# Kernel optimization log

Hardware: AMD Instinct MI355X
Metric: run time of the kernel (lower is better)

The kernel has to match this reference:

```python
import jax, jax.numpy as jnp
import numpy as np

ROPE_BASE = 10000.0

def _rope(x, positions):
    # x: [B, H, T, hs], rotate-half (GPT-NeoX style) rotary embedding
    hs = x.shape[-1]
    half = hs // 2
    inv_freq = 1.0 / (ROPE_BASE ** (jnp.arange(half, dtype=jnp.float32) / half))
    ang = positions.astype(jnp.float32)[:, None] * inv_freq[None, :]  # [T, half]
    cos, sin = jnp.cos(ang), jnp.sin(ang)
    x1, x2 = x[..., :half], x[..., half:]
    return jnp.concatenate([x1 * cos - x2 * sin, x1 * sin + x2 * cos], axis=-1)


def setup_inputs() -> dict:
    key = jax.random.key(0)
    ks = jax.random.split(key, 8)
    B, T, OFF, C, H = 1, 1024, 1024, 2048, 16
    hs = C // H
    return {
        "x": jax.random.normal(ks[0], (B, T, C), jnp.float32),
        "cached_k": jax.random.normal(ks[1], (B, H, OFF, hs), jnp.float32),
        "cached_v": jax.random.normal(ks[2], (B, H, OFF, hs), jnp.float32),
        "W_attn": jax.random.normal(ks[3], (C, 3 * C), jnp.float32) * 0.02,
        "b_attn": jnp.zeros((3 * C,), jnp.float32),
        "W_proj": jax.random.normal(ks[4], (C, C), jnp.float32) * 0.02,
        "b_proj": jnp.zeros((C,), jnp.float32),
        "decay_raw": jax.random.normal(ks[5], (16,), jnp.float32) * 0.5,
    }


def reference(x, cached_k, cached_v, W_attn, b_attn, W_proj, b_proj, decay_raw):
    B, T, C = x.shape
    H = decay_raw.shape[0]
    hs = C // H
    off = cached_k.shape[2]

    qkv = x @ W_attn + b_attn                       # [B, T, 3C]
    q, k, v = jnp.split(qkv, 3, axis=-1)
    to_heads = lambda t: t.reshape(B, T, H, hs).transpose(0, 2, 1, 3)  # [B,H,T,hs]
    q, k, v = to_heads(q), to_heads(k), to_heads(v)

    positions = jnp.arange(off, off + T)
    q = _rope(q, positions)
    k = _rope(k, positions)

    k = jnp.concatenate([cached_k, k], axis=2)      # [B, H, T_full, hs]
    v = jnp.concatenate([cached_v, v], axis=2)
    T_full = k.shape[2]

    # causal mask over full key length, offset for cache
    neg_inf = jnp.finfo(jnp.float32).min
    q_idx = positions                               # [T]
    k_idx = jnp.arange(T_full)                      # [T_full]
    causal = jnp.where(k_idx[None, :] > q_idx[:, None], neg_inf, 0.0)  # [T, T_full]

    # per-head distance-decay log-bias
    decay = jax.nn.softplus(decay_raw)              # [H]
    dist = jnp.maximum(q_idx[:, None] - k_idx[None, :], 0).astype(jnp.float32)
    logw = -jnp.log1p(decay[:, None, None] * jnp.log1p(dist))          # [H, T, T_full]
    bias = causal[None, :, :] + logw                # [H, T, T_full]

    scale = 1.0 / jnp.sqrt(jnp.float32(hs))
    scores = jnp.einsum('bhtd,bhsd->bhts', q, k) * scale + bias[None]
    attn = jax.nn.softmax(scores, axis=-1)
    y = jnp.einsum('bhts,bhsd->bhtd', attn, v)      # [B, H, T, hs]
    y = y.transpose(0, 2, 1, 3).reshape(B, T, C)
    y = y @ W_proj + b_proj
    return (y, k, v)
```

## Files before the change

kernel.cpp:

```cpp
#include <hip/hip_runtime.h>
#include <hip/hip_bf16.h>

typedef unsigned short u16;
typedef unsigned int u32;
typedef __attribute__((ext_vector_type(4))) float f32x4;
typedef __attribute__((ext_vector_type(8))) short bf16x8;

__device__ __forceinline__ u16 f2bf(float f) {
    union { float f; u32 u; } v; v.f = f;
    return (u16)((v.u + 0x7FFFu + ((v.u >> 16) & 1u)) >> 16);
}
__device__ __forceinline__ float bf2f(u16 b) {
    union { u32 u; float f; } v; v.u = ((u32)b) << 16;
    return v.f;
}
__device__ __forceinline__ void st_out(float* p, float v) { *p = v; }
__device__ __forceinline__ void st_out(u16* p, float v) { *p = f2bf(v); }

__device__ __forceinline__ f32x4 mfma16(bf16x8 a, bf16x8 b, f32x4 c) {
    return __builtin_amdgcn_mfma_f32_16x16x32_bf16(a, b, c, 0, 0, 0);
}

#define GLD_LDS16(g, l) __builtin_amdgcn_global_load_lds( \
    (const __attribute__((address_space(1))) void*)(g),   \
    (__attribute__((address_space(3))) void*)(l), 16, 0, 0)

__global__ __launch_bounds__(256) void k_prep(
    const float* __restrict__ W_attn, const float* __restrict__ W_proj,
    const float* __restrict__ x, const float* __restrict__ decay_raw,
    u16* __restrict__ WaT, u16* __restrict__ WpT, u16* __restrict__ Xb,
    float* __restrict__ bias_tab, float* __restrict__ cosT, float* __restrict__ sinT) {
    __shared__ float tile[64][65];
    const int b = blockIdx.x, tid = threadIdx.x;
    if (b < 4096) {
        const float* src; u16* dst; int R, Cc, bx, by;
        if (b < 3072) { src = W_attn; dst = WaT; R = 2048; Cc = 6144; bx = b % 96; by = b / 96; }
        else          { src = W_proj; dst = WpT; R = 2048; Cc = 2048; bx = (b - 3072) & 31; by = (b - 3072) >> 5; }
        int c0 = bx * 64, r0 = by * 64;
#pragma unroll
        for (int it = 0; it < 16; ++it) {
            int idx = it * 256 + tid;
            int r = idx >> 6, c = idx & 63;
            tile[r][c] = src[(size_t)(r0 + r) * Cc + c0 + c];
        }
        __syncthreads();
#pragma unroll
        for (int it = 0; it < 16; ++it) {
            int idx = it * 256 + tid;
            int cc = idx >> 6, rr = idx & 63;
            dst[(size_t)(c0 + cc) * R + r0 + rr] = f2bf(tile[rr][cc]);
        }
    } else if (b < 6144) {
        int i = (b - 4096) * 256 + tid;
        float4 v = ((const float4*)x)[i];
        u32 p0 = (u32)f2bf(v.x) | ((u32)f2bf(v.y) << 16);
        u32 p1 = (u32)f2bf(v.z) | ((u32)f2bf(v.w) << 16);
        uint2 p; p.x = p0; p.y = p1;
        *(uint2*)(Xb + (size_t)i * 4) = p;
    } else {
        int i = (b - 6144) * 256 + tid;
        if (i < 16 * 2048) {
            int h = i >> 11, dist = i & 2047;
            float dec = log1pf(expf(decay_raw[h]));
            bias_tab[i] = -log1pf(dec * log1pf((float)dist));
        }
        if (i < 1024 * 64) {
            int t = i >> 6, j = i & 63;
            float inv = expf(-logf(10000.0f) * (float)j / 64.0f);
            float ang = (float)(1024 + t) * inv;
            cosT[i] = cosf(ang);
            sinT[i] = sinf(ang);
        }
    }
}

template<int BM, int BN, int WRG, int WCG, typename OT>
__global__ __launch_bounds__(256) void k_gemm_bt(
    const u16* __restrict__ A, const u16* __restrict__ Bt,
    const float* __restrict__ bias, OT* __restrict__ C,
    int M, int N, int K) {
    constexpr int BK = 64;
    constexpr int WM = BM / WRG;
    constexpr int WN = BN / WCG;
    constexpr int MR = WM / 16;
    constexpr int NR = WN / 16;
    constexpr int LDSZ = (BM + BN) * BK * 2;
    __shared__ char lds[2][LDSZ];

    const int tid = threadIdx.x;
    const int lane = tid & 63, wid = tid >> 6;
    const int wr = wid / WCG, wc = wid % WCG;
    const int lhi = lane >> 4, llo = lane & 15;
    const int m0 = blockIdx.y * BM, n0 = blockIdx.x * BN;

    f32x4 acc[MR][NR];
#pragma unroll
    for (int m = 0; m < MR; ++m)
#pragma unroll
        for (int n = 0; n < NR; ++n)
            acc[m][n] = f32x4{0.f, 0.f, 0.f, 0.f};

    auto stage = [&](int buf, int k0) {
        char* ldsA = &lds[buf][0];
        char* ldsB = &lds[buf][0] + BM * BK * 2;
#pragma unroll
        for (int it = 0; it < (BM * 8) / 256; ++it) {
            int ci = it * 256 + wid * 64 + lane;
            int r = ci >> 3, c = ci & 7;
            int sc = c ^ (r & 7);
            GLD_LDS16(A + (size_t)(m0 + r) * K + k0 + sc * 8,
                      ldsA + (it * 256 + wid * 64) * 16);
        }
#pragma unroll
        for (int it = 0; it < (BN * 8) / 256; ++it) {
            int ci = it * 256 + wid * 64 + lane;
            int r = ci >> 3, c = ci & 7;
            int sc = c ^ (r & 7);
            GLD_LDS16(Bt + (size_t)(n0 + r) * K + k0 + sc * 8,
                      ldsB + (it * 256 + wid * 64) * 16);
        }
    };

    stage(0, 0);
    __syncthreads();
    int cur = 0;
    for (int k0 = 0; k0 < K; k0 += BK) {
        if (k0 + BK < K) stage(cur ^ 1, k0 + BK);
        const char* ldsA = &lds[cur][0];
        const char* ldsB = &lds[cur][0] + BM * BK * 2;
#pragma unroll
        for (int kk = 0; kk < BK; kk += 32) {
            bf16x8 af[MR], bfr[NR];
            const int clb = (kk >> 3) + lhi;
#pragma unroll
            for (int m = 0; m < MR; ++m) {
                int row = wr * WM + m * 16 + llo;
                af[m] = *(const bf16x8*)(ldsA + row * 128 + ((clb ^ (row & 7)) << 4));
            }
#pragma unroll
            for (int n = 0; n < NR; ++n) {
                int row = wc * WN + n * 16 + llo;
                bfr[n] = *(const bf16x8*)(ldsB + row * 128 + ((clb ^ (row & 7)) << 4));
            }
#pragma unroll
            for (int m = 0; m < MR; ++m)
#pragma unroll
                for (int n = 0; n < NR; ++n)
                    acc[m][n] = mfma16(af[m], bfr[n], acc[m][n]);
        }
        __syncthreads();
        cur ^= 1;
    }
#pragma unroll
    for (int m = 0; m < MR; ++m) {
        int row = m0 + wr * WM + m * 16 + lhi * 4;
#pragma unroll
        for (int n = 0; n < NR; ++n) {
            int col = n0 + wc * WN + n * 16 + llo;
            float bv = bias[col];
#pragma unroll
            for (int j = 0; j < 4; ++j)
                st_out(&C[(size_t)(row + j) * N + col], acc[m][n][j] + bv);
        }
    }
}

__global__ void k_fuse2(const u16* __restrict__ qkv,
                        const float* __restrict__ cosT, const float* __restrict__ sinT,
                        const float* __restrict__ cached_k,
                        u16* __restrict__ qb, u16* __restrict__ kb,
                        float* __restrict__ out_k) {
    const int b = blockIdx.x;
    if (b < 4096) {
        int i = b * 256 + threadIdx.x;
        int j = i & 63;
        int t = (i >> 6) & 1023;
        int h = i >> 16;
        const u16* row = qkv + (size_t)t * 6144;
        float q1 = bf2f(row[h * 128 + j]),        q2 = bf2f(row[h * 128 + j + 64]);
        float k1 = bf2f(row[2048 + h * 128 + j]), k2 = bf2f(row[2048 + h * 128 + j + 64]);
        float cv = cosT[t * 64 + j], sv = sinT[t * 64 + j];
        float qo1 = q1 * cv - q2 * sv, qo2 = q1 * sv + q2 * cv;
        float ko1 = k1 * cv - k2 * sv, ko2 = k1 * sv + k2 * cv;
        size_t qoff = ((size_t)h * 1024 + t) * 128 + j;
        qb[qoff] = f2bf(qo1); qb[qoff + 64] = f2bf(qo2);
        size_t koff = ((size_t)h * 2048 + 1024 + t) * 128 + j;
        kb[koff] = f2bf(ko1); kb[koff + 64] = f2bf(ko2);
        out_k[koff] = ko1; out_k[koff + 64] = ko2;
    } else {
        int i = (b - 4096) * 256 + threadIdx.x;
        int d = i & 127, s = (i >> 7) & 1023, h = i >> 17;
        float v = cached_k[i];
        size_t off = ((size_t)h * 2048 + s) * 128 + d;
        out_k[off] = v;
        kb[off] = f2bf(v);
    }
}

__global__ __launch_bounds__(256) void k_v_assemble(
    const float* __restrict__ cached_v, const u16* __restrict__ qkv,
    float* __restrict__ out_v, u16* __restrict__ vt) {
    __shared__ u16 tile[64][65];
    int s0 = blockIdx.x * 64, d0 = blockIdx.y * 64, h = blockIdx.z;
    int tid = threadIdx.x;
#pragma unroll
    for (int it = 0; it < 16; ++it) {
        int idx = it * 256 + tid;
        int r = idx >> 6, c = idx & 63;
        int s = s0 + r, d = d0 + c;
        u16 v = (s < 1024)
            ? f2bf(cached_v[((size_t)h * 1024 + s) * 128 + d])
            : qkv[(size_t)(s - 1024) * 6144 + 4096 + h * 128 + d];
        tile[r][c] = v;
        out_v[((size_t)h * 2048 + s) * 128 + d] = bf2f(v);
    }
    __syncthreads();
#pragma unroll
    for (int it = 0; it < 16; ++it) {
        int idx = it * 256 + tid;
        int dd = idx >> 6, ss = idx & 63;
        vt[((size_t)h * 128 + d0 + dd) * 2048 + s0 + ss] = tile[ss][dd];
    }
}

__global__ __launch_bounds__(256, 4) void k_attn(
    const u16* __restrict__ qb,
    const u16* __restrict__ kb,
    const u16* __restrict__ vt,
    const float* __restrict__ bias_tab,
    u16* __restrict__ Pacc,
    float* __restrict__ Pm,
    float* __restrict__ Pl) {
    __shared__ char ldsK[2][32 * 256];
    __shared__ char ldsV[2][128 * 64];
    __shared__ u16 ldsP[4][16 * 36];

    const int bid = blockIdx.x;
    const int xcd = bid & 7, idx = bid >> 3;
    const int work = xcd * 128 + idx;
    const int h = work >> 6, rem = work & 63;
    const int qt = rem >> 2, chunk = rem & 3;
    const int qbase = qt * 64;
    const int tid = threadIdx.x, lane = tid & 63, wid = tid >> 6;
    const int lhi = lane >> 4, llo = lane & 15;
    const int slot = (h * 16 + qt) * 4 + chunk;

    const u16* kg = kb + (size_t)h * 2048 * 128;
    const u16* vg = vt + (size_t)h * 128 * 2048;
    const float* bt = bias_tab + h * 2048;

    bf16x8 qf[4];
    {
        const u16* qrow = qb + ((size_t)h * 1024 + qbase + wid * 16 + llo) * 128;
#pragma unroll
        for (int c = 0; c < 4; ++c)
            qf[c] = *(const bf16x8*)(qrow + c * 32 + lhi * 8);
    }

    f32x4 acc[8];
#pragma unroll
    for (int d = 0; d < 8; ++d) acc[d] = f32x4{0.f, 0.f, 0.f, 0.f};
    float mrow[4] = {-3e38f, -3e38f, -3e38f, -3e38f};
    float lrow[4] = {0.f, 0.f, 0.f, 0.f};

    const int ntiles = 34 + 2 * qt;
    const float scale = 0.08838834764831845f;
    const int qpos = 1024 + qbase + wid * 16 + lhi * 4;

    auto stage = [&](int b, int st) {
        int sbase = st * 32;
#pragma unroll
        for (int it = 0; it < 2; ++it) {
            int ci = it * 256 + tid;
            int r = ci >> 4, c = ci & 15;
            int sc = c ^ (r & 7);
            GLD_LDS16(kg + (size_t)(sbase + r) * 128 + sc * 8,
                      &ldsK[b][0] + (it * 256 + wid * 64) * 16);
        }
#pragma unroll
        for (int it = 0; it < 2; ++it) {
            int ci = it * 256 + tid;
            int r = ci >> 2, c = ci & 3;
            int sc = c ^ ((r >> 1) & 3);
            GLD_LDS16(vg + (size_t)r * 2048 + sbase + sc * 8,
                      &ldsV[b][0] + (it * 256 + wid * 64) * 16);
        }
    };

    const int st0 = chunk + 4 * ((ntiles - 1 - chunk) >> 2);
    stage(0, st0);
    __syncthreads();
    int cur = 0;
    for (int st = st0; st >= chunk; st -= 4) {
        if (st >= chunk + 4) stage(cur ^ 1, st - 4);
        const int sbase = st * 32;
        const char* lK = &ldsK[cur][0];
        const char* lV = &ldsV[cur][0];

        f32x4 sc4[2];
        __builtin_amdgcn_s_setprio(1);
#pragma unroll
        for (int sub = 0; sub < 2; ++sub) {
            f32x4 s4 = f32x4{0.f, 0.f, 0.f, 0.f};
            int key = sub * 16 + llo;
#pragma unroll
            for (int c2 = 0; c2 < 4; ++c2) {
                int cl = c2 * 4 + lhi;
                bf16x8 kf = *(const bf16x8*)(lK + key * 256 + ((cl ^ (key & 7)) << 4));
                s4 = mfma16(qf[c2], kf, s4);
            }
            sc4[sub] = s4;
        }
        __builtin_amdgcn_s_setprio(0);

#pragma unroll
        for (int sub = 0; sub < 2; ++sub) {
            int key = sbase + sub * 16 + llo;
#pragma unroll
            for (int j = 0; j < 4; ++j) {
                int dist = qpos + j - key;
                float bv = bt[dist < 0 ? 0 : dist];
                sc4[sub][j] = (dist < 0) ? -3e38f : sc4[sub][j] * scale + bv;
            }
        }
        float tmax[4];
        int ok = 1;
#pragma unroll
        for (int j = 0; j < 4; ++j) {
            tmax[j] = fmaxf(sc4[0][j], sc4[1][j]);
            ok &= (tmax[j] <= mrow[j] + 8.0f) ? 1 : 0;
        }
        if (!__all(ok)) {
#pragma unroll
            for (int j = 0; j < 4; ++j) {
                float t = tmax[j];
                t = fmaxf(t, __shfl_xor(t, 1));
                t = fmaxf(t, __shfl_xor(t, 2));
                t = fmaxf(t, __shfl_xor(t, 4));
                t = fmaxf(t, __shfl_xor(t, 8));
                float mnew = fmaxf(mrow[j], t);
                float fs = __expf(mrow[j] - mnew);
                mrow[j] = mnew;
                lrow[j] *= fs;
#pragma unroll
                for (int d = 0; d < 8; ++d) acc[d][j] *= fs;
            }
        }
#pragma unroll
        for (int sub = 0; sub < 2; ++sub)
#pragma unroll
            for (int j = 0; j < 4; ++j) {
                float p = __expf(sc4[sub][j] - mrow[j]);
                sc4[sub][j] = p;
                lrow[j] += p;
            }

        u16* P = &ldsP[wid][0];
#pragma unroll
        for (int sub = 0; sub < 2; ++sub)
#pragma unroll
            for (int j = 0; j < 4; ++j)
                P[(lhi * 4 + j) * 36 + sub * 16 + llo] = f2bf(sc4[sub][j]);

        bf16x8 pf = *(const bf16x8*)((const char*)P + llo * 72 + lhi * 16);
        __builtin_amdgcn_s_setprio(1);
#pragma unroll
        for (int db = 0; db < 8; ++db) {
            int dr = db * 16 + llo;
            int cl = lhi ^ ((dr >> 1) & 3);
            bf16x8 vf = *(const bf16x8*)(lV + dr * 64 + cl * 16);
            acc[db] = mfma16(pf, vf, acc[db]);
        }
        __builtin_amdgcn_s_setprio(0);
        __syncthreads();
        cur ^= 1;
    }

#pragma unroll
    for (int j = 0; j < 4; ++j) {
        float t = lrow[j];
        t += __shfl_xor(t, 1);
        t += __shfl_xor(t, 2);
        t += __shfl_xor(t, 4);
        t += __shfl_xor(t, 8);
        lrow[j] = t;
    }

    if (llo == 0) {
#pragma unroll
        for (int j = 0; j < 4; ++j) {
            int r = wid * 16 + lhi * 4 + j;
            Pm[(size_t)slot * 64 + r] = mrow[j];
            Pl[(size_t)slot * 64 + r] = lrow[j];
        }
    }
#pragma unroll
    for (int db = 0; db < 8; ++db)
#pragma unroll
        for (int j = 0; j < 4; ++j) {
            int r = wid * 16 + lhi * 4 + j;
            Pacc[(size_t)slot * 8192 + r * 128 + db * 16 + llo] = f2bf(acc[db][j]);
        }
}

__global__ __launch_bounds__(256) void k_merge(
    const u16* __restrict__ Pacc, const float* __restrict__ Pm,
    const float* __restrict__ Pl, u16* __restrict__ yb) {
    const int b = blockIdx.x;
    const int h = b >> 6, qt = (b >> 2) & 15, quarter = b & 3;
    const int slot0 = (h * 16 + qt) * 4;
    const int tid = threadIdx.x;
    const int r = tid >> 2, dd = (tid & 3) * 8 + quarter * 32;

    float m[4], l[4];
#pragma unroll
    for (int c = 0; c < 4; ++c) {
        m[c] = Pm[(size_t)(slot0 + c) * 64 + r];
        l[c] = Pl[(size_t)(slot0 + c) * 64 + r];
    }
    float M = fmaxf(fmaxf(m[0], m[1]), fmaxf(m[2], m[3]));
    float w[4], L = 0.f;
#pragma unroll
    for (int c = 0; c < 4; ++c) {
        w[c] = __expf(m[c] - M);
        L += w[c] * l[c];
    }
    float inv = 1.0f / L;

    float y[8];
#pragma unroll
    for (int i = 0; i < 8; ++i) y[i] = 0.f;
#pragma unroll
    for (int c = 0; c < 4; ++c) {
        const uint4* pa = (const uint4*)(Pacc + (size_t)(slot0 + c) * 8192 + r * 128 + dd);
        float wc = w[c];
        uint4 v = *pa;
        u32 a[4] = {v.x, v.y, v.z, v.w};
#pragma unroll
        for (int p = 0; p < 4; ++p) {
            y[p * 2]     += wc * bf2f((u16)(a[p] & 0xFFFF));
            y[p * 2 + 1] += wc * bf2f((u16)(a[p] >> 16));
        }
    }
    int trow = qt * 64 + r;
    uint4 outv;
    u32* ow = (u32*)&outv;
#pragma unroll
    for (int k = 0; k < 4; ++k)
        ow[k] = (u32)f2bf(y[2 * k] * inv) | ((u32)f2bf(y[2 * k + 1] * inv) << 16);
    *(uint4*)(yb + (size_t)trow * 2048 + h * 128 + dd) = outv;
}

extern "C" void kernel_launch(void* const* d_in, const int* in_sizes, int n_in,
                              void* d_out, int out_size, void* d_ws, size_t ws_size,
                              hipStream_t stream) {
    (void)in_sizes; (void)n_in; (void)out_size;
    const float* x         = (const float*)d_in[0];
    const float* cached_k  = (const float*)d_in[1];
    const float* cached_v  = (const float*)d_in[2];
    const float* W_attn    = (const float*)d_in[3];
    const float* b_attn    = (const float*)d_in[4];
    const float* W_proj    = (const float*)d_in[5];
    const float* b_proj    = (const float*)d_in[6];
    const float* decay_raw = (const float*)d_in[7];

    float* out_y = (float*)d_out;
    float* out_k = out_y + 2097152;
    float* out_v = out_y + 6291456;

    char* ws = (char*)d_ws;
    if (ws_size < 63569920) return;
    u16*   WaT  = (u16*)(ws);
    u16*   WpT  = (u16*)(ws + 25165824);
    u16*   Xb   = (u16*)(ws + 33554432);
    u16*   QKVb = (u16*)(ws + 37748736);
    float* BT   = (float*)(ws + 62914560);
    float* CT   = (float*)(ws + 63045632);
    float* ST   = (float*)(ws + 63307776);
    u16*   Qb   = (u16*)(ws);
    u16*   Kb   = (u16*)(ws + 4194304);
    u16*   Vt   = (u16*)(ws + 12582912);
    u16*   Yb   = (u16*)(ws + 20971520);
    float* Pm   = (float*)(ws + 33554432);
    float* Pl   = (float*)(ws + 33816576);
    u16*   Pacc = (u16*)(ws + 37748736);

    k_prep<<<6400, 256, 0, stream>>>(W_attn, W_proj, x, decay_raw, WaT, WpT, Xb, BT, CT, ST);
    k_gemm_bt<128, 64, 2, 2, u16><<<dim3(96, 8), 256, 0, stream>>>(Xb, WaT, b_attn, QKVb, 1024, 6144, 2048);
    k_fuse2<<<12288, 256, 0, stream>>>(QKVb, CT, ST, cached_k, Qb, Kb, out_k);
    k_v_assemble<<<dim3(32, 2, 16), 256, 0, stream>>>(cached_v, QKVb, out_v, Vt);
    k_attn<<<1024, 256, 0, stream>>>(Qb, Kb, Vt, BT, Pacc, Pm, Pl);
    k_merge<<<1024, 256, 0, stream>>>(Pacc, Pm, Pl, Yb);
    k_gemm_bt<64, 64, 2, 2, float><<<dim3(32, 16), 256, 0, stream>>>(Yb, WpT, b_proj, out_y, 1024, 2048, 2048);
}
```

Baseline: 139.4 us.

## Split attention into six key chunks, fold scale into Q, prefetch bias, use exp2

The attention kernel now splits each query tile's key range into six interleaved chunks instead of four, launching 1536 blocks for more parallelism, and the merge kernel combines six partials. The softmax scale and log2(e) are folded into Q in the rope kernel and into the bias table, so the inner loop uses exp2f and skips a multiply. Bias values for fully unmasked tiles are prefetched one iteration ahead as vector loads instead of being gathered per element, and the rescale threshold is adjusted for the base-2 domain. The extra chunks add more partial-result traffic and merge work, and the Pl workspace offset moves to fit the larger Pm.

```diff
diff --git a/kernel.cpp b/kernel.cpp
--- a/kernel.cpp
+++ b/kernel.cpp
@@ -4,6 +4,7 @@
 typedef unsigned short u16;
 typedef unsigned int u32;
 typedef __attribute__((ext_vector_type(4))) float f32x4;
+typedef float f32x4u __attribute__((ext_vector_type(4), aligned(4)));
 typedef __attribute__((ext_vector_type(8))) short bf16x8;
 
 __device__ __forceinline__ u16 f2bf(float f) {
@@ -24,6 +25,9 @@
 #define GLD_LDS16(g, l) __builtin_amdgcn_global_load_lds( \
     (const __attribute__((address_space(1))) void*)(g),   \
     (__attribute__((address_space(3))) void*)(l), 16, 0, 0)
+
+#define LOG2E 1.4426950408889634f
+#define QSCALE 0.12751743f
 
 __global__ __launch_bounds__(256) void k_prep(
     const float* __restrict__ W_attn, const float* __restrict__ W_proj,
@@ -62,7 +66,7 @@
         if (i < 16 * 2048) {
             int h = i >> 11, dist = i & 2047;
             float dec = log1pf(expf(decay_raw[h]));
-            bias_tab[i] = -log1pf(dec * log1pf((float)dist));
+            bias_tab[i] = -log1pf(dec * log1pf((float)dist)) * LOG2E;
         }
         if (i < 1024 * 64) {
             int t = i >> 6, j = i & 63;
@@ -183,7 +187,7 @@
         float qo1 = q1 * cv - q2 * sv, qo2 = q1 * sv + q2 * cv;
         float ko1 = k1 * cv - k2 * sv, ko2 = k1 * sv + k2 * cv;
         size_t qoff = ((size_t)h * 1024 + t) * 128 + j;
-        qb[qoff] = f2bf(qo1); qb[qoff + 64] = f2bf(qo2);
+        qb[qoff] = f2bf(qo1 * QSCALE); qb[qoff + 64] = f2bf(qo2 * QSCALE);
         size_t koff = ((size_t)h * 2048 + 1024 + t) * 128 + j;
         kb[koff] = f2bf(ko1); kb[koff + 64] = f2bf(ko2);
         out_k[koff] = ko1; out_k[koff + 64] = ko2;
@@ -237,13 +241,13 @@
 
     const int bid = blockIdx.x;
     const int xcd = bid & 7, idx = bid >> 3;
-    const int work = xcd * 128 + idx;
-    const int h = work >> 6, rem = work & 63;
-    const int qt = rem >> 2, chunk = rem & 3;
+    const int work = xcd * 192 + idx;
+    const int h = work / 96, rem = work % 96;
+    const int qt = rem / 6, chunk = rem % 6;
     const int qbase = qt * 64;
     const int tid = threadIdx.x, lane = tid & 63, wid = tid >> 6;
     const int lhi = lane >> 4, llo = lane & 15;
-    const int slot = (h * 16 + qt) * 4 + chunk;
+    const int slot = (h * 16 + qt) * 6 + chunk;
 
     const u16* kg = kb + (size_t)h * 2048 * 128;
     const u16* vg = vt + (size_t)h * 128 * 2048;
@@ -264,7 +268,6 @@
     float lrow[4] = {0.f, 0.f, 0.f, 0.f};
 
     const int ntiles = 34 + 2 * qt;
-    const float scale = 0.08838834764831845f;
     const int qpos = 1024 + qbase + wid * 16 + lhi * 4;
 
     auto stage = [&](int b, int st) {
@@ -287,15 +290,26 @@
         }
     };
 
-    const int st0 = chunk + 4 * ((ntiles - 1 - chunk) >> 2);
+    f32x4u bpre0, bpre1;
+    auto pf_bias = [&](int st) {
+        int d0 = qpos - (st * 32 + llo);
+        int d1 = d0 - 16;
+        bpre0 = *(const f32x4u*)(bt + (d0 < 0 ? 0 : d0));
+        bpre1 = *(const f32x4u*)(bt + (d1 < 0 ? 0 : d1));
+    };
+
+    const int st0 = chunk + 6 * ((ntiles - 1 - chunk) / 6);
     stage(0, st0);
+    pf_bias(st0);
     __syncthreads();
     int cur = 0;
-    for (int st = st0; st >= chunk; st -= 4) {
-        if (st >= chunk + 4) stage(cur ^ 1, st - 4);
+    for (int st = st0; st >= chunk; st -= 6) {
+        if (st >= chunk + 6) stage(cur ^ 1, st - 6);
         const int sbase = st * 32;
         const char* lK = &ldsK[cur][0];
         const char* lV = &ldsV[cur][0];
+        f32x4u bc0 = bpre0, bc1 = bpre1;
+        if (st >= chunk + 6) pf_bias(st - 6);
 
         f32x4 sc4[2];
         __builtin_amdgcn_s_setprio(1);
@@ -313,14 +327,22 @@
         }
         __builtin_amdgcn_s_setprio(0);
 
-#pragma unroll
-        for (int sub = 0; sub < 2; ++sub) {
-            int key = sbase + sub * 16 + llo;
+        if (sbase + 31 <= 1024 + qbase + wid * 16) {
 #pragma unroll
             for (int j = 0; j < 4; ++j) {
-                int dist = qpos + j - key;
-                float bv = bt[dist < 0 ? 0 : dist];
-                sc4[sub][j] = (dist < 0) ? -3e38f : sc4[sub][j] * scale + bv;
+                sc4[0][j] += bc0[j];
+                sc4[1][j] += bc1[j];
+            }
+        } else {
+#pragma unroll
+            for (int sub = 0; sub < 2; ++sub) {
+                int key = sbase + sub * 16 + llo;
+#pragma unroll
+                for (int j = 0; j < 4; ++j) {
+                    int dist = qpos + j - key;
+                    float bv = bt[dist < 0 ? 0 : dist];
+                    sc4[sub][j] = (dist < 0) ? -3e38f : sc4[sub][j] + bv;
+                }
             }
         }
         float tmax[4];
@@ -328,7 +350,7 @@
 #pragma unroll
         for (int j = 0; j < 4; ++j) {
             tmax[j] = fmaxf(sc4[0][j], sc4[1][j]);
-            ok &= (tmax[j] <= mrow[j] + 8.0f) ? 1 : 0;
+            ok &= (tmax[j] <= mrow[j] + 11.5416f) ? 1 : 0;
         }
         if (!__all(ok)) {
 #pragma unroll
@@ -339,7 +361,7 @@
                 t = fmaxf(t, __shfl_xor(t, 4));
                 t = fmaxf(t, __shfl_xor(t, 8));
                 float mnew = fmaxf(mrow[j], t);
-                float fs = __expf(mrow[j] - mnew);
+                float fs = exp2f(mrow[j] - mnew);
                 mrow[j] = mnew;
                 lrow[j] *= fs;
 #pragma unroll
@@ -350,7 +372,7 @@
         for (int sub = 0; sub < 2; ++sub)
 #pragma unroll
             for (int j = 0; j < 4; ++j) {
-                float p = __expf(sc4[sub][j] - mrow[j]);
+                float p = exp2f(sc4[sub][j] - mrow[j]);
                 sc4[sub][j] = p;
                 lrow[j] += p;
             }
@@ -408,21 +430,23 @@
     const float* __restrict__ Pl, u16* __restrict__ yb) {
     const int b = blockIdx.x;
     const int h = b >> 6, qt = (b >> 2) & 15, quarter = b & 3;
-    const int slot0 = (h * 16 + qt) * 4;
+    const int slot0 = (h * 16 + qt) * 6;
     const int tid = threadIdx.x;
     const int r = tid >> 2, dd = (tid & 3) * 8 + quarter * 32;
 
-    float m[4], l[4];
-#pragma unroll
-    for (int c = 0; c < 4; ++c) {
+    float m[6], l[6];
+#pragma unroll
+    for (int c = 0; c < 6; ++c) {
         m[c] = Pm[(size_t)(slot0 + c) * 64 + r];
         l[c] = Pl[(size_t)(slot0 + c) * 64 + r];
     }
-    float M = fmaxf(fmaxf(m[0], m[1]), fmaxf(m[2], m[3]));
-    float w[4], L = 0.f;
-#pragma unroll
-    for (int c = 0; c < 4; ++c) {
-        w[c] = __expf(m[c] - M);
+    float M = m[0];
+#pragma unroll
+    for (int c = 1; c < 6; ++c) M = fmaxf(M, m[c]);
+    float w[6], L = 0.f;
+#pragma unroll
+    for (int c = 0; c < 6; ++c) {
+        w[c] = exp2f(m[c] - M);
         L += w[c] * l[c];
     }
     float inv = 1.0f / L;
@@ -431,7 +455,7 @@
 #pragma unroll
     for (int i = 0; i < 8; ++i) y[i] = 0.f;
 #pragma unroll
-    for (int c = 0; c < 4; ++c) {
+    for (int c = 0; c < 6; ++c) {
         const uint4* pa = (const uint4*)(Pacc + (size_t)(slot0 + c) * 8192 + r * 128 + dd);
         float wc = w[c];
         uint4 v = *pa;
@@ -482,14 +506,14 @@
     u16*   Vt   = (u16*)(ws + 12582912);
     u16*   Yb   = (u16*)(ws + 20971520);
     float* Pm   = (float*)(ws + 33554432);
-    float* Pl   = (float*)(ws + 33816576);
+    float* Pl   = (float*)(ws + 33947648);
     u16*   Pacc = (u16*)(ws + 37748736);
 
     k_prep<<<6400, 256, 0, stream>>>(W_attn, W_proj, x, decay_raw, WaT, WpT, Xb, BT, CT, ST);
     k_gemm_bt<128, 64, 2, 2, u16><<<dim3(96, 8), 256, 0, stream>>>(Xb, WaT, b_attn, QKVb, 1024, 6144, 2048);
     k_fuse2<<<12288, 256, 0, stream>>>(QKVb, CT, ST, cached_k, Qb, Kb, out_k);
     k_v_assemble<<<dim3(32, 2, 16), 256, 0, stream>>>(cached_v, QKVb, out_v, Vt);
-    k_attn<<<1024, 256, 0, stream>>>(Qb, Kb, Vt, BT, Pacc, Pm, Pl);
+    k_attn<<<1536, 256, 0, stream>>>(Qb, Kb, Vt, BT, Pacc, Pm, Pl);
     k_merge<<<1024, 256, 0, stream>>>(Pacc, Pm, Pl, Yb);
     k_gemm_bt<64, 64, 2, 2, float><<<dim3(32, 16), 256, 0, stream>>>(Yb, WpT, b_proj, out_y, 1024, 2048, 2048);
 }
```

Result: no change. 142.2 us (+2.0%).

## Restructure attention kernel to two-wave blocks with transposed QK and register P

Applied to the files above, without the earlier changes.

The attention kernel now runs 128-thread blocks where each wave handles 32 query rows (two 16-row MFMA tiles). This reuses each K/V fragment loaded from LDS across two MFMAs. QK^T is computed transposed so each lane owns a query row, and P is packed to bf16 in registers and permuted with cross-lane shuffles instead of going through LDS. The softmax scale and log2e are folded into Q and the bias table so exp2 can be used, and fully unmasked tiles load the distance bias as vectors. The cost is higher register pressure and fewer waves per block, which could reduce occupancy.

```diff
diff --git a/kernel.cpp b/kernel.cpp
--- a/kernel.cpp
+++ b/kernel.cpp
@@ -4,6 +4,7 @@
 typedef unsigned short u16;
 typedef unsigned int u32;
 typedef __attribute__((ext_vector_type(4))) float f32x4;
+typedef float f32x4u __attribute__((ext_vector_type(4), aligned(4)));
 typedef __attribute__((ext_vector_type(8))) short bf16x8;
 
 __device__ __forceinline__ u16 f2bf(float f) {
@@ -20,10 +21,18 @@
 __device__ __forceinline__ f32x4 mfma16(bf16x8 a, bf16x8 b, f32x4 c) {
     return __builtin_amdgcn_mfma_f32_16x16x32_bf16(a, b, c, 0, 0, 0);
 }
+__device__ __forceinline__ u32 cvt_pk_bf16(float lo, float hi) {
+    u32 r;
+    asm("v_cvt_pk_bf16_f32 %0, %1, %2" : "=v"(r) : "v"(lo), "v"(hi));
+    return r;
+}
 
 #define GLD_LDS16(g, l) __builtin_amdgcn_global_load_lds( \
     (const __attribute__((address_space(1))) void*)(g),   \
     (__attribute__((address_space(3))) void*)(l), 16, 0, 0)
+
+#define LOG2E 1.4426950408889634f
+#define QSCALE 0.12751743f
 
 __global__ __launch_bounds__(256) void k_prep(
     const float* __restrict__ W_attn, const float* __restrict__ W_proj,
@@ -62,7 +71,7 @@
         if (i < 16 * 2048) {
             int h = i >> 11, dist = i & 2047;
             float dec = log1pf(expf(decay_raw[h]));
-            bias_tab[i] = -log1pf(dec * log1pf((float)dist));
+            bias_tab[i] = -log1pf(dec * log1pf((float)dist)) * LOG2E;
         }
         if (i < 1024 * 64) {
             int t = i >> 6, j = i & 63;
@@ -183,7 +192,7 @@
         float qo1 = q1 * cv - q2 * sv, qo2 = q1 * sv + q2 * cv;
         float ko1 = k1 * cv - k2 * sv, ko2 = k1 * sv + k2 * cv;
         size_t qoff = ((size_t)h * 1024 + t) * 128 + j;
-        qb[qoff] = f2bf(qo1); qb[qoff + 64] = f2bf(qo2);
+        qb[qoff] = f2bf(qo1 * QSCALE); qb[qoff + 64] = f2bf(qo2 * QSCALE);
         size_t koff = ((size_t)h * 2048 + 1024 + t) * 128 + j;
         kb[koff] = f2bf(ko1); kb[koff + 64] = f2bf(ko2);
         out_k[koff] = ko1; out_k[koff + 64] = ko2;
@@ -223,7 +232,7 @@
     }
 }
 
-__global__ __launch_bounds__(256, 4) void k_attn(
+__global__ __launch_bounds__(128, 2) void k_attn(
     const u16* __restrict__ qb,
     const u16* __restrict__ kb,
     const u16* __restrict__ vt,
@@ -233,7 +242,6 @@
     float* __restrict__ Pl) {
     __shared__ char ldsK[2][32 * 256];
     __shared__ char ldsV[2][128 * 64];
-    __shared__ u16 ldsP[4][16 * 36];
 
     const int bid = blockIdx.x;
     const int xcd = bid & 7, idx = bid >> 3;
@@ -249,42 +257,59 @@
     const u16* vg = vt + (size_t)h * 128 * 2048;
     const float* bt = bias_tab + h * 2048;
 
-    bf16x8 qf[4];
-    {
-        const u16* qrow = qb + ((size_t)h * 1024 + qbase + wid * 16 + llo) * 128;
+    bf16x8 qf[2][4];
+#pragma unroll
+    for (int m = 0; m < 2; ++m) {
+        const u16* qrow = qb + ((size_t)h * 1024 + qbase + wid * 32 + m * 16 + llo) * 128;
 #pragma unroll
         for (int c = 0; c < 4; ++c)
-            qf[c] = *(const bf16x8*)(qrow + c * 32 + lhi * 8);
-    }
-
-    f32x4 acc[8];
-#pragma unroll
-    for (int d = 0; d < 8; ++d) acc[d] = f32x4{0.f, 0.f, 0.f, 0.f};
-    float mrow[4] = {-3e38f, -3e38f, -3e38f, -3e38f};
-    float lrow[4] = {0.f, 0.f, 0.f, 0.f};
+            qf[m][c] = *(const bf16x8*)(qrow + c * 32 + lhi * 8);
+    }
+
+    f32x4 acc[2][8];
+#pragma unroll
+    for (int m = 0; m < 2; ++m)
+#pragma unroll
+        for (int d = 0; d < 8; ++d) acc[m][d] = f32x4{0.f, 0.f, 0.f, 0.f};
+    float mrow[2] = {-3e38f, -3e38f};
+    float lrow[2] = {0.f, 0.f};
 
     const int ntiles = 34 + 2 * qt;
-    const float scale = 0.08838834764831845f;
-    const int qpos = 1024 + qbase + wid * 16 + lhi * 4;
+    const int qpos0 = 1024 + qbase + wid * 32 + llo;
 
     auto stage = [&](int b, int st) {
         int sbase = st * 32;
 #pragma unroll
-        for (int it = 0; it < 2; ++it) {
-            int ci = it * 256 + tid;
+        for (int it = 0; it < 4; ++it) {
+            int ci = it * 128 + tid;
             int r = ci >> 4, c = ci & 15;
             int sc = c ^ (r & 7);
             GLD_LDS16(kg + (size_t)(sbase + r) * 128 + sc * 8,
-                      &ldsK[b][0] + (it * 256 + wid * 64) * 16);
-        }
-#pragma unroll
-        for (int it = 0; it < 2; ++it) {
-            int ci = it * 256 + tid;
+                      &ldsK[b][0] + (it * 128 + wid * 64) * 16);
+        }
+#pragma unroll
+        for (int it = 0; it < 4; ++it) {
+            int ci = it * 128 + tid;
             int r = ci >> 2, c = ci & 3;
             int sc = c ^ ((r >> 1) & 3);
             GLD_LDS16(vg + (size_t)r * 2048 + sbase + sc * 8,
-                      &ldsV[b][0] + (it * 256 + wid * 64) * 16);
-        }
+                      &ldsV[b][0] + (it * 128 + wid * 64) * 16);
+        }
+    };
+
+    auto permP = [&](u32 p0, u32 p1, u32 p2, u32 p3) -> bf16x8 {
+        u32 r16a = (u32)__shfl_xor((int)(lhi == 1 ? p0 : p2), 16);
+        u32 r16b = (u32)__shfl_xor((int)(lhi == 1 ? p1 : p3), 16);
+        u32 r32a = (u32)__shfl_xor((int)(lhi == 3 ? p0 : p2), 32);
+        u32 r32b = (u32)__shfl_xor((int)(lhi == 3 ? p1 : p3), 32);
+        u32 r48a = (u32)__shfl_xor((int)(lhi == 2 ? p0 : p2), 48);
+        u32 r48b = (u32)__shfl_xor((int)(lhi == 2 ? p1 : p3), 48);
+        union { u32 w[4]; bf16x8 v; } u;
+        u.w[0] = lhi == 0 ? p0 : lhi == 1 ? r48a : lhi == 2 ? r32a : r16a;
+        u.w[1] = lhi == 0 ? p1 : lhi == 1 ? r48b : lhi == 2 ? r32b : r16b;
+        u.w[2] = lhi == 0 ? r16a : lhi == 1 ? r32a : lhi == 2 ? r48a : p2;
+        u.w[3] = lhi == 0 ? r16b : lhi == 1 ? r32b : lhi == 2 ? r48b : p3;
+        return u.v;
     };
 
     const int st0 = chunk + 4 * ((ntiles - 1 - chunk) >> 2);
@@ -297,79 +322,111 @@
         const char* lK = &ldsK[cur][0];
         const char* lV = &ldsV[cur][0];
 
-        f32x4 sc4[2];
+        const int D0 = qpos0 - sbase - lhi * 4;
+        f32x4u wB = *(const f32x4u*)(bt + (D0 - 3 < 0 ? 0 : D0 - 3));
+        f32x4u wA = *(const f32x4u*)(bt + (D0 + 13 < 0 ? 0 : D0 + 13));
+        f32x4u wC = *(const f32x4u*)(bt + (D0 - 19 < 0 ? 0 : D0 - 19));
+
+        f32x4 sc4[2][2];
         __builtin_amdgcn_s_setprio(1);
 #pragma unroll
         for (int sub = 0; sub < 2; ++sub) {
-            f32x4 s4 = f32x4{0.f, 0.f, 0.f, 0.f};
+            f32x4 a0 = f32x4{0.f, 0.f, 0.f, 0.f};
+            f32x4 a1 = f32x4{0.f, 0.f, 0.f, 0.f};
             int key = sub * 16 + llo;
 #pragma unroll
             for (int c2 = 0; c2 < 4; ++c2) {
                 int cl = c2 * 4 + lhi;
                 bf16x8 kf = *(const bf16x8*)(lK + key * 256 + ((cl ^ (key & 7)) << 4));
-                s4 = mfma16(qf[c2], kf, s4);
+                a0 = mfma16(kf, qf[0][c2], a0);
+                a1 = mfma16(kf, qf[1][c2], a1);
             }
-            sc4[sub] = s4;
+            sc4[0][sub] = a0;
+            sc4[1][sub] = a1;
         }
         __builtin_amdgcn_s_setprio(0);
 
-#pragma unroll
-        for (int sub = 0; sub < 2; ++sub) {
-            int key = sbase + sub * 16 + llo;
+        if (sbase + 31 <= 1024 + qbase + wid * 32) {
 #pragma unroll
             for (int j = 0; j < 4; ++j) {
-                int dist = qpos + j - key;
-                float bv = bt[dist < 0 ? 0 : dist];
-                sc4[sub][j] = (dist < 0) ? -3e38f : sc4[sub][j] * scale + bv;
+                sc4[0][0][j] += wB[3 - j];
+                sc4[0][1][j] += wC[3 - j];
+                sc4[1][0][j] += wA[3 - j];
+                sc4[1][1][j] += wB[3 - j];
             }
-        }
-        float tmax[4];
+        } else {
+#pragma unroll
+            for (int m = 0; m < 2; ++m)
+#pragma unroll
+                for (int sub = 0; sub < 2; ++sub)
+#pragma unroll
+                    for (int j = 0; j < 4; ++j) {
+                        int key = sbase + sub * 16 + lhi * 4 + j;
+                        int dist = qpos0 + m * 16 - key;
+                        float bv = bt[dist < 0 ? 0 : dist];
+                        sc4[m][sub][j] = (dist < 0) ? -3e38f : sc4[m][sub][j] + bv;
+                    }
+        }
+
+        float tmax[2];
         int ok = 1;
 #pragma unroll
-        for (int j = 0; j < 4; ++j) {
-            tmax[j] = fmaxf(sc4[0][j], sc4[1][j]);
-            ok &= (tmax[j] <= mrow[j] + 8.0f) ? 1 : 0;
+        for (int m = 0; m < 2; ++m) {
+            float t = fmaxf(fmaxf(fmaxf(sc4[m][0][0], sc4[m][0][1]),
+                                  fmaxf(sc4[m][0][2], sc4[m][0][3])),
+                            fmaxf(fmaxf(sc4[m][1][0], sc4[m][1][1]),
+                                  fmaxf(sc4[m][1][2], sc4[m][1][3])));
+            tmax[m] = t;
+            ok &= (t <= mrow[m] + 11.5416f) ? 1 : 0;
         }
         if (!__all(ok)) {
 #pragma unroll
-            for (int j = 0; j < 4; ++j) {
-                float t = tmax[j];
-                t = fmaxf(t, __shfl_xor(t, 1));
-                t = fmaxf(t, __shfl_xor(t, 2));
-                t = fmaxf(t, __shfl_xor(t, 4));
-                t = fmaxf(t, __shfl_xor(t, 8));
-                float mnew = fmaxf(mrow[j], t);
-                float fs = __expf(mrow[j] - mnew);
-                mrow[j] = mnew;
-                lrow[j] *= fs;
-#pragma unroll
-                for (int d = 0; d < 8; ++d) acc[d][j] *= fs;
+            for (int m = 0; m < 2; ++m) {
+                float t = tmax[m];
+                t = fmaxf(t, __shfl_xor(t, 16));
+                t = fmaxf(t, __shfl_xor(t, 32));
+                float mnew = fmaxf(mrow[m], t);
+                float fs = exp2f(mrow[m] - mnew);
+                mrow[m] = mnew;
+                lrow[m] *= fs;
+                float fsj[4];
+#pragma unroll
+                for (int j = 0; j < 4; ++j)
+                    fsj[j] = __shfl(fs, ((lane >> 4) << 2) + j);
+#pragma unroll
+                for (int d = 0; d < 8; ++d)
+#pragma unroll
+                    for (int j = 0; j < 4; ++j) acc[m][d][j] *= fsj[j];
             }
         }
-#pragma unroll
-        for (int sub = 0; sub < 2; ++sub)
-#pragma unroll
-            for (int j = 0; j < 4; ++j) {
-                float p = __expf(sc4[sub][j] - mrow[j]);
-                sc4[sub][j] = p;
-                lrow[j] += p;
-            }
-
-        u16* P = &ldsP[wid][0];
-#pragma unroll
-        for (int sub = 0; sub < 2; ++sub)
-#pragma unroll
-            for (int j = 0; j < 4; ++j)
-                P[(lhi * 4 + j) * 36 + sub * 16 + llo] = f2bf(sc4[sub][j]);
-
-        bf16x8 pf = *(const bf16x8*)((const char*)P + llo * 72 + lhi * 16);
+
+        bf16x8 pa[2];
+#pragma unroll
+        for (int m = 0; m < 2; ++m) {
+            float p[8];
+#pragma unroll
+            for (int sub = 0; sub < 2; ++sub)
+#pragma unroll
+                for (int j = 0; j < 4; ++j) {
+                    float e = exp2f(sc4[m][sub][j] - mrow[m]);
+                    lrow[m] += e;
+                    p[sub * 4 + j] = e;
+                }
+            u32 pk0 = cvt_pk_bf16(p[0], p[1]);
+            u32 pk1 = cvt_pk_bf16(p[2], p[3]);
+            u32 pk2 = cvt_pk_bf16(p[4], p[5]);
+            u32 pk3 = cvt_pk_bf16(p[6], p[7]);
+            pa[m] = permP(pk0, pk1, pk2, pk3);
+        }
+
         __builtin_amdgcn_s_setprio(1);
 #pragma unroll
         for (int db = 0; db < 8; ++db) {
             int dr = db * 16 + llo;
             int cl = lhi ^ ((dr >> 1) & 3);
             bf16x8 vf = *(const bf16x8*)(lV + dr * 64 + cl * 16);
-            acc[db] = mfma16(pf, vf, acc[db]);
+            acc[0][db] = mfma16(pa[0], vf, acc[0][db]);
+            acc[1][db] = mfma16(pa[1], vf, acc[1][db]);
         }
         __builtin_amdgcn_s_setprio(0);
         __syncthreads();
@@ -377,30 +434,30 @@
     }
 
 #pragma unroll
-    for (int j = 0; j < 4; ++j) {
-        float t = lrow[j];
-        t += __shfl_xor(t, 1);
-        t += __shfl_xor(t, 2);
-        t += __shfl_xor(t, 4);
-        t += __shfl_xor(t, 8);
-        lrow[j] = t;
-    }
-
-    if (llo == 0) {
-#pragma unroll
-        for (int j = 0; j < 4; ++j) {
-            int r = wid * 16 + lhi * 4 + j;
-            Pm[(size_t)slot * 64 + r] = mrow[j];
-            Pl[(size_t)slot * 64 + r] = lrow[j];
-        }
-    }
-#pragma unroll
-    for (int db = 0; db < 8; ++db)
-#pragma unroll
-        for (int j = 0; j < 4; ++j) {
-            int r = wid * 16 + lhi * 4 + j;
-            Pacc[(size_t)slot * 8192 + r * 128 + db * 16 + llo] = f2bf(acc[db][j]);
-        }
+    for (int m = 0; m < 2; ++m) {
+        float t = lrow[m];
+        t += __shfl_xor(t, 16);
+        t += __shfl_xor(t, 32);
+        lrow[m] = t;
+    }
+
+    if (lhi == 0) {
+#pragma unroll
+        for (int m = 0; m < 2; ++m) {
+            int r = wid * 32 + m * 16 + llo;
+            Pm[(size_t)slot * 64 + r] = mrow[m];
+            Pl[(size_t)slot * 64 + r] = lrow[m];
+        }
+    }
+#pragma unroll
+    for (int m = 0; m < 2; ++m)
+#pragma unroll
+        for (int db = 0; db < 8; ++db)
+#pragma unroll
+            for (int j = 0; j < 4; ++j) {
+                int r = wid * 32 + m * 16 + lhi * 4 + j;
+                Pacc[(size_t)slot * 8192 + r * 128 + db * 16 + llo] = f2bf(acc[m][db][j]);
+            }
 }
 
 __global__ __launch_bounds__(256) void k_merge(
@@ -422,7 +479,7 @@
     float w[4], L = 0.f;
 #pragma unroll
     for (int c = 0; c < 4; ++c) {
-        w[c] = __expf(m[c] - M);
+        w[c] = exp2f(m[c] - M);
         L += w[c] * l[c];
     }
     float inv = 1.0f / L;
@@ -489,7 +546,7 @@
     k_gemm_bt<128, 64, 2, 2, u16><<<dim3(96, 8), 256, 0, stream>>>(Xb, WaT, b_attn, QKVb, 1024, 6144, 2048);
     k_fuse2<<<12288, 256, 0, stream>>>(QKVb, CT, ST, cached_k, Qb, Kb, out_k);
     k_v_assemble<<<dim3(32, 2, 16), 256, 0, stream>>>(cached_v, QKVb, out_v, Vt);
-    k_attn<<<1024, 256, 0, stream>>>(Qb, Kb, Vt, BT, Pacc, Pm, Pl);
+    k_attn<<<1024, 128, 0, stream>>>(Qb, Kb, Vt, BT, Pacc, Pm, Pl);
     k_merge<<<1024, 256, 0, stream>>>(Pacc, Pm, Pl, Yb);
     k_gemm_bt<64, 64, 2, 2, float><<<dim3(32, 16), 256, 0, stream>>>(Yb, WpT, b_proj, out_y, 1024, 2048, 2048);
 }
```

New measurement: 140.7 us. No clear change (+0.9%).

## Transpose QK MFMA to keep P in registers and use exp2 softmax

Applied to the files above, without the earlier changes.

Swaps the operands of the QK^T MFMA so each lane holds one query row. Row max and sum then need only cross-group shuffles, and the P matrix is rebuilt for the PV MFMA with lane shuffles and packed bf16 converts instead of an LDS round trip. The softmax scale and log2e are folded into Q and the bias table so exp2 can be used. Unmasked tiles load the bias as contiguous vector reads instead of per-element gathers. The shuffle-based permutation adds VALU and cross-lane work, and prescaling Q before bf16 rounding slightly changes numerics.

```diff
diff --git a/kernel.cpp b/kernel.cpp
--- a/kernel.cpp
+++ b/kernel.cpp
@@ -4,6 +4,7 @@
 typedef unsigned short u16;
 typedef unsigned int u32;
 typedef __attribute__((ext_vector_type(4))) float f32x4;
+typedef float f32x4u __attribute__((ext_vector_type(4), aligned(4)));
 typedef __attribute__((ext_vector_type(8))) short bf16x8;
 
 __device__ __forceinline__ u16 f2bf(float f) {
@@ -20,10 +21,18 @@
 __device__ __forceinline__ f32x4 mfma16(bf16x8 a, bf16x8 b, f32x4 c) {
     return __builtin_amdgcn_mfma_f32_16x16x32_bf16(a, b, c, 0, 0, 0);
 }
+__device__ __forceinline__ u32 cvt_pk_bf16(float lo, float hi) {
+    u32 r;
+    asm("v_cvt_pk_bf16_f32 %0, %1, %2" : "=v"(r) : "v"(lo), "v"(hi));
+    return r;
+}
 
 #define GLD_LDS16(g, l) __builtin_amdgcn_global_load_lds( \
     (const __attribute__((address_space(1))) void*)(g),   \
     (__attribute__((address_space(3))) void*)(l), 16, 0, 0)
+
+#define LOG2E 1.4426950408889634f
+#define QSCALE 0.12751743f
 
 __global__ __launch_bounds__(256) void k_prep(
     const float* __restrict__ W_attn, const float* __restrict__ W_proj,
@@ -62,7 +71,7 @@
         if (i < 16 * 2048) {
             int h = i >> 11, dist = i & 2047;
             float dec = log1pf(expf(decay_raw[h]));
-            bias_tab[i] = -log1pf(dec * log1pf((float)dist));
+            bias_tab[i] = -log1pf(dec * log1pf((float)dist)) * LOG2E;
         }
         if (i < 1024 * 64) {
             int t = i >> 6, j = i & 63;
@@ -183,7 +192,7 @@
         float qo1 = q1 * cv - q2 * sv, qo2 = q1 * sv + q2 * cv;
         float ko1 = k1 * cv - k2 * sv, ko2 = k1 * sv + k2 * cv;
         size_t qoff = ((size_t)h * 1024 + t) * 128 + j;
-        qb[qoff] = f2bf(qo1); qb[qoff + 64] = f2bf(qo2);
+        qb[qoff] = f2bf(qo1 * QSCALE); qb[qoff + 64] = f2bf(qo2 * QSCALE);
         size_t koff = ((size_t)h * 2048 + 1024 + t) * 128 + j;
         kb[koff] = f2bf(ko1); kb[koff + 64] = f2bf(ko2);
         out_k[koff] = ko1; out_k[koff + 64] = ko2;
@@ -233,7 +242,6 @@
     float* __restrict__ Pl) {
     __shared__ char ldsK[2][32 * 256];
     __shared__ char ldsV[2][128 * 64];
-    __shared__ u16 ldsP[4][16 * 36];
 
     const int bid = blockIdx.x;
     const int xcd = bid & 7, idx = bid >> 3;
@@ -260,12 +268,11 @@
     f32x4 acc[8];
 #pragma unroll
     for (int d = 0; d < 8; ++d) acc[d] = f32x4{0.f, 0.f, 0.f, 0.f};
-    float mrow[4] = {-3e38f, -3e38f, -3e38f, -3e38f};
-    float lrow[4] = {0.f, 0.f, 0.f, 0.f};
+    float mrow = -3e38f;
+    float lrow = 0.f;
 
     const int ntiles = 34 + 2 * qt;
-    const float scale = 0.08838834764831845f;
-    const int qpos = 1024 + qbase + wid * 16 + lhi * 4;
+    const int qpos = 1024 + qbase + wid * 16 + llo;
 
     auto stage = [&](int b, int st) {
         int sbase = st * 32;
@@ -285,6 +292,21 @@
             GLD_LDS16(vg + (size_t)r * 2048 + sbase + sc * 8,
                       &ldsV[b][0] + (it * 256 + wid * 64) * 16);
         }
+    };
+
+    auto permP = [&](u32 p0, u32 p1, u32 p2, u32 p3) -> bf16x8 {
+        u32 r16a = (u32)__shfl_xor((int)(lhi == 1 ? p0 : p2), 16);
+        u32 r16b = (u32)__shfl_xor((int)(lhi == 1 ? p1 : p3), 16);
+        u32 r32a = (u32)__shfl_xor((int)(lhi == 3 ? p0 : p2), 32);
+        u32 r32b = (u32)__shfl_xor((int)(lhi == 3 ? p1 : p3), 32);
+        u32 r48a = (u32)__shfl_xor((int)(lhi == 2 ? p0 : p2), 48);
+        u32 r48b = (u32)__shfl_xor((int)(lhi == 2 ? p1 : p3), 48);
+        union { u32 w[4]; bf16x8 v; } u;
+        u.w[0] = lhi == 0 ? p0 : lhi == 1 ? r48a : lhi == 2 ? r32a : r16a;
+        u.w[1] = lhi == 0 ? p1 : lhi == 1 ? r48b : lhi == 2 ? r32b : r16b;
+        u.w[2] = lhi == 0 ? r16a : lhi == 1 ? r32a : lhi == 2 ? r48a : p2;
+        u.w[3] = lhi == 0 ? r16b : lhi == 1 ? r32b : lhi == 2 ? r48b : p3;
+        return u.v;
     };
 
     const int st0 = chunk + 4 * ((ntiles - 1 - chunk) >> 2);
@@ -297,6 +319,10 @@
         const char* lK = &ldsK[cur][0];
         const char* lV = &ldsV[cur][0];
 
+        const int D0 = qpos - sbase - lhi * 4;
+        f32x4u wB = *(const f32x4u*)(bt + (D0 - 3 < 0 ? 0 : D0 - 3));
+        f32x4u wC = *(const f32x4u*)(bt + (D0 - 19 < 0 ? 0 : D0 - 19));
+
         f32x4 sc4[2];
         __builtin_amdgcn_s_setprio(1);
 #pragma unroll
@@ -307,92 +333,87 @@
             for (int c2 = 0; c2 < 4; ++c2) {
                 int cl = c2 * 4 + lhi;
                 bf16x8 kf = *(const bf16x8*)(lK + key * 256 + ((cl ^ (key & 7)) << 4));
-                s4 = mfma16(qf[c2], kf, s4);
+                s4 = mfma16(kf, qf[c2], s4);
             }
             sc4[sub] = s4;
         }
         __builtin_amdgcn_s_setprio(0);
 
-#pragma unroll
-        for (int sub = 0; sub < 2; ++sub) {
-            int key = sbase + sub * 16 + llo;
+        if (sbase + 31 <= 1024 + qbase + wid * 16) {
 #pragma unroll
             for (int j = 0; j < 4; ++j) {
-                int dist = qpos + j - key;
-                float bv = bt[dist < 0 ? 0 : dist];
-                sc4[sub][j] = (dist < 0) ? -3e38f : sc4[sub][j] * scale + bv;
+                sc4[0][j] += wB[3 - j];
+                sc4[1][j] += wC[3 - j];
             }
-        }
-        float tmax[4];
-        int ok = 1;
-#pragma unroll
-        for (int j = 0; j < 4; ++j) {
-            tmax[j] = fmaxf(sc4[0][j], sc4[1][j]);
-            ok &= (tmax[j] <= mrow[j] + 8.0f) ? 1 : 0;
-        }
+        } else {
+#pragma unroll
+            for (int sub = 0; sub < 2; ++sub)
+#pragma unroll
+                for (int j = 0; j < 4; ++j) {
+                    int key = sbase + sub * 16 + lhi * 4 + j;
+                    int dist = qpos - key;
+                    float bv = bt[dist < 0 ? 0 : dist];
+                    sc4[sub][j] = (dist < 0) ? -3e38f : sc4[sub][j] + bv;
+                }
+        }
+
+        float tmax = fmaxf(fmaxf(fmaxf(sc4[0][0], sc4[0][1]), fmaxf(sc4[0][2], sc4[0][3])),
+                           fmaxf(fmaxf(sc4[1][0], sc4[1][1]), fmaxf(sc4[1][2], sc4[1][3])));
+        int ok = (tmax <= mrow + 11.5416f) ? 1 : 0;
         if (!__all(ok)) {
+            float t = tmax;
+            t = fmaxf(t, __shfl_xor(t, 16));
+            t = fmaxf(t, __shfl_xor(t, 32));
+            float mnew = fmaxf(mrow, t);
+            float fs = exp2f(mrow - mnew);
+            mrow = mnew;
+            lrow *= fs;
+            float fsj[4];
+#pragma unroll
+            for (int j = 0; j < 4; ++j)
+                fsj[j] = __shfl(fs, lhi * 4 + j);
+#pragma unroll
+            for (int d = 0; d < 8; ++d)
+#pragma unroll
+                for (int j = 0; j < 4; ++j) acc[d][j] *= fsj[j];
+        }
+
+        float p[8];
+#pragma unroll
+        for (int sub = 0; sub < 2; ++sub)
 #pragma unroll
             for (int j = 0; j < 4; ++j) {
-                float t = tmax[j];
-                t = fmaxf(t, __shfl_xor(t, 1));
-                t = fmaxf(t, __shfl_xor(t, 2));
-                t = fmaxf(t, __shfl_xor(t, 4));
-                t = fmaxf(t, __shfl_xor(t, 8));
-                float mnew = fmaxf(mrow[j], t);
-                float fs = __expf(mrow[j] - mnew);
-                mrow[j] = mnew;
-                lrow[j] *= fs;
-#pragma unroll
-                for (int d = 0; d < 8; ++d) acc[d][j] *= fs;
+                float e = exp2f(sc4[sub][j] - mrow);
+                lrow += e;
+                p[sub * 4 + j] = e;
             }
-        }
-#pragma unroll
-        for (int sub = 0; sub < 2; ++sub)
-#pragma unroll
-            for (int j = 0; j < 4; ++j) {
-                float p = __expf(sc4[sub][j] - mrow[j]);
-                sc4[sub][j] = p;
-                lrow[j] += p;
-            }
-
-        u16* P = &ldsP[wid][0];
-#pragma unroll
-        for (int sub = 0; sub < 2; ++sub)
-#pragma unroll
-            for (int j = 0; j < 4; ++j)
-                P[(lhi * 4 + j) * 36 + sub * 16 + llo] = f2bf(sc4[sub][j]);
-
-        bf16x8 pf = *(const bf16x8*)((const char*)P + llo * 72 + lhi * 16);
+        bf16x8 pa = permP(cvt_pk_bf16(p[0], p[1]), cvt_pk_bf16(p[2], p[3]),
+                          cvt_pk_bf16(p[4], p[5]), cvt_pk_bf16(p[6], p[7]));
+
         __builtin_amdgcn_s_setprio(1);
 #pragma unroll
         for (int db = 0; db < 8; ++db) {
             int dr = db * 16 + llo;
             int cl = lhi ^ ((dr >> 1) & 3);
             bf16x8 vf = *(const bf16x8*)(lV + dr * 64 + cl * 16);
-            acc[db] = mfma16(pf, vf, acc[db]);
+            acc[db] = mfma16(pa, vf, acc[db]);
         }
         __builtin_amdgcn_s_setprio(0);
         __syncthreads();
         cur ^= 1;
     }
 
-#pragma unroll
-    for (int j = 0; j < 4; ++j) {
-        float t = lrow[j];
-        t += __shfl_xor(t, 1);
-        t += __shfl_xor(t, 2);
-        t += __shfl_xor(t, 4);
-        t += __shfl_xor(t, 8);
-        lrow[j] = t;
-    }
-
-    if (llo == 0) {
-#pragma unroll
-        for (int j = 0; j < 4; ++j) {
-            int r = wid * 16 + lhi * 4 + j;
-            Pm[(size_t)slot * 64 + r] = mrow[j];
-            Pl[(size_t)slot * 64 + r] = lrow[j];
-        }
+    {
+        float t = lrow;
+        t += __shfl_xor(t, 16);
+        t += __shfl_xor(t, 32);
+        lrow = t;
+    }
+
+    if (lhi == 0) {
+        int r = wid * 16 + llo;
+        Pm[(size_t)slot * 64 + r] = mrow;
+        Pl[(size_t)slot * 64 + r] = lrow;
     }
 #pragma unroll
     for (int db = 0; db < 8; ++db)
@@ -422,7 +443,7 @@
     float w[4], L = 0.f;
 #pragma unroll
     for (int c = 0; c < 4; ++c) {
-        w[c] = __expf(m[c] - M);
+        w[c] = exp2f(m[c] - M);
         L += w[c] * l[c];
     }
     float inv = 1.0f / L;
```

New measurement: 135.3 us. 2.9% less time.
